# Kernel optimization log

Measured on AMD Instinct MI355X. Metric: run time of the kernel, lower is better.

The kernel has to match this reference:

```python
import jax, jax.numpy as jnp
import numpy as np

EPS = 1e-8  # torch F.cosine_similarity eps
TEMP = 2.0  # hardcoded in module regardless of init arg


def _normalize(x):
    # row-normalize with torch-style eps clamp on the norm
    norm = jnp.sqrt(jnp.sum(x * x, axis=-1, keepdims=True))
    return x / jnp.maximum(norm, EPS)


def setup_inputs() -> dict:
    key = jax.random.key(0)
    k1, k2, k3 = jax.random.split(key, 3)
    n, m, d = 8192, 8192, 256
    return {
        "pos_key": jax.random.normal(k1, (n, d), dtype=jnp.float32),
        "pos_value": jax.random.normal(k2, (n, d), dtype=jnp.float32),
        "neg_value": jax.random.normal(k3, (m, d), dtype=jnp.float32),
    }


def reference(pos_key, pos_value, neg_value):
    pk = _normalize(pos_key)    # [n, d]
    pv = _normalize(pos_value)  # [n, d]
    nv = _normalize(neg_value)  # [m, d]

    pos_sim = jnp.sum(pk * pv, axis=-1)          # [n]
    neg_sim = jnp.einsum("nd,md->nm", pk, nv)    # [n, m] cosine sims

    pos_loss = -jnp.mean(pos_sim / TEMP)
    # log-sum-exp over m (stable), matching log(sum(exp(.)))
    neg_loss = jnp.mean(jax.scipy.special.logsumexp(neg_sim / TEMP, axis=-1))
    return pos_loss + neg_loss
```

## Files before the change

### kernel.cpp

```cpp
#include <hip/hip_runtime.h>

typedef __attribute__((ext_vector_type(4))) float f32x4;
typedef __attribute__((ext_vector_type(4))) int   i32x4;
typedef __attribute__((ext_vector_type(8))) int   i32x8;

#define DIM 256
#define D4  64

#define GLD_LDS16(g, l) __builtin_amdgcn_global_load_lds(                      \
    (const __attribute__((address_space(1))) void*)(g),                        \
    (__attribute__((address_space(3))) void*)(l), 16, 0, 0)

__global__ __launch_bounds__(256) void normalize_kernel(
    const float4* __restrict__ pk, const float4* __restrict__ pv,
    const float4* __restrict__ nv, unsigned int* __restrict__ pkn,
    unsigned int* __restrict__ nvn, float* __restrict__ posPart, int N) {
  int row  = blockIdx.x * 4 + (threadIdx.x >> 6);
  int lane = threadIdx.x & 63;
  if (row < N) {
    float4 x = pk[row * D4 + lane];
    float4 y = pv[row * D4 + lane];
    float skk = x.x*x.x + x.y*x.y + x.z*x.z + x.w*x.w;
    float svv = y.x*y.x + y.y*y.y + y.z*y.z + y.w*y.w;
    float skv = x.x*y.x + x.y*y.y + x.z*y.z + x.w*y.w;
#pragma unroll
    for (int m = 32; m >= 1; m >>= 1) {
      skk += __shfl_xor(skk, m, 64);
      svv += __shfl_xor(svv, m, 64);
      skv += __shfl_xor(skv, m, 64);
    }
    float nk  = fmaxf(sqrtf(skk), 1e-8f);
    float nvv = fmaxf(sqrtf(svv), 1e-8f);
    if (lane == 0) posPart[row] = skv / (nk * nvv);
    float rk = 1.0f / nk;
    int w = __builtin_amdgcn_cvt_pk_fp8_f32(x.x * rk, x.y * rk, 0, false);
    w = __builtin_amdgcn_cvt_pk_fp8_f32(x.z * rk, x.w * rk, w, true);
    pkn[(size_t)row * 64 + lane] = (unsigned int)w;
  } else {
    int r2 = row - N;
    float4 x = nv[r2 * D4 + lane];
    float s = x.x*x.x + x.y*x.y + x.z*x.z + x.w*x.w;
#pragma unroll
    for (int m = 32; m >= 1; m >>= 1) s += __shfl_xor(s, m, 64);
    float rn = 1.0f / fmaxf(sqrtf(s), 1e-8f);
    int w = __builtin_amdgcn_cvt_pk_fp8_f32(x.x * rn, x.y * rn, 0, false);
    w = __builtin_amdgcn_cvt_pk_fp8_f32(x.z * rn, x.w * rn, w, true);
    nvn[(size_t)r2 * 64 + lane] = (unsigned int)w;
  }
}

__global__ __launch_bounds__(256, 3) void gemm_lse_kernel(
    const unsigned char* __restrict__ gA, const unsigned char* __restrict__ gB,
    float* __restrict__ partial, int N) {
  __shared__ unsigned char As[16384];
  __shared__ unsigned char Bs[16384];

  const int tid  = threadIdx.x;
  const int lane = tid & 63;
  const int wv   = tid >> 6;
  const int wm   = wv >> 1, wn = wv & 1;
  const int l15  = lane & 15, q = lane >> 4;
  const int row0 = blockIdx.y * 128;
  const int col0 = blockIdx.x * 128;
  const float kLog2eHalf = 0.72134752044448170f;
  const int kUnitScale = 0x7F7F7F7F;

  f32x4 acc[4][4];
#pragma unroll
  for (int mi = 0; mi < 4; mi++)
#pragma unroll
    for (int ni = 0; ni < 4; ni++) acc[mi][ni] = (f32x4){0.f, 0.f, 0.f, 0.f};

#pragma unroll
  for (int kb = 0; kb < 2; kb++) {
    if (kb) __syncthreads();
#pragma unroll
    for (int i = 0; i < 4; i++) {
      int c  = i * 256 + tid;
      int r  = c >> 3;
      int sc = ((c & 7) ^ (r & 7)) << 4;
      GLD_LDS16(gA + (size_t)(row0 + r) * 256 + kb * 128 + sc, As + c * 16);
      GLD_LDS16(gB + (size_t)(col0 + r) * 256 + kb * 128 + sc, Bs + c * 16);
    }
    __syncthreads();

    i32x8 bf[4];
#pragma unroll
    for (int ni = 0; ni < 4; ni++) {
      int r  = wn * 64 + ni * 16 + l15;
      int c0 = (q * 2)     ^ (r & 7);
      int c1 = (q * 2 + 1) ^ (r & 7);
      i32x4 lo = *(const i32x4*)(Bs + r * 128 + c0 * 16);
      i32x4 hi = *(const i32x4*)(Bs + r * 128 + c1 * 16);
      bf[ni] = (i32x8){lo.x, lo.y, lo.z, lo.w, hi.x, hi.y, hi.z, hi.w};
    }
#pragma unroll
    for (int mi = 0; mi < 4; mi++) {
      int r  = wm * 64 + mi * 16 + l15;
      int c0 = (q * 2)     ^ (r & 7);
      int c1 = (q * 2 + 1) ^ (r & 7);
      i32x4 lo = *(const i32x4*)(As + r * 128 + c0 * 16);
      i32x4 hi = *(const i32x4*)(As + r * 128 + c1 * 16);
      i32x8 af = (i32x8){lo.x, lo.y, lo.z, lo.w, hi.x, hi.y, hi.z, hi.w};
#pragma unroll
      for (int ni = 0; ni < 4; ni++)
        acc[mi][ni] = __builtin_amdgcn_mfma_scale_f32_16x16x128_f8f6f4(
            af, bf[ni], acc[mi][ni],
            0, 0, 0, kUnitScale, 0, kUnitScale);
    }
  }

  float keep = 0.f;
#pragma unroll
  for (int mi = 0; mi < 4; mi++)
#pragma unroll
    for (int rr = 0; rr < 4; rr++) {
      float v = 0.f;
#pragma unroll
      for (int ni = 0; ni < 4; ni++)
        v += __builtin_amdgcn_exp2f(acc[mi][ni][rr] * kLog2eHalf);
      v += __shfl_xor(v, 1, 16);
      v += __shfl_xor(v, 2, 16);
      v += __shfl_xor(v, 4, 16);
      v += __shfl_xor(v, 8, 16);
      if (l15 == mi * 4 + rr) keep = v;
    }
  int lrow = (l15 >> 2) * 16 + q * 4 + (l15 & 3);
  partial[(size_t)(blockIdx.x * 2 + wn) * N + row0 + wm * 64 + lrow] = keep;
}

__global__ __launch_bounds__(256) void finalize_kernel(
    const float* __restrict__ partial, const float* __restrict__ posPart,
    float* __restrict__ out, int N, int slabsPerGroup, float invN) {
  __shared__ float red[4][64];
  int t  = threadIdx.x;
  int rl = t & 63, g = t >> 6;
  int row = blockIdx.x * 64 + rl;
  const float* p = partial + (size_t)(g * slabsPerGroup) * N + row;
  float s = 0.f;
#pragma unroll 8
  for (int j = 0; j < slabsPerGroup; j++) s += p[(size_t)j * N];
  red[g][rl] = s;
  __syncthreads();
  if (t < 64) {
    float tot = red[0][rl] + red[1][rl] + red[2][rl] + red[3][rl];
    float v = __builtin_amdgcn_logf(tot) * 0.69314718055994531f
              - 0.5f * posPart[row];
#pragma unroll
    for (int m = 32; m >= 1; m >>= 1) v += __shfl_xor(v, m, 64);
    if (rl == 0) atomicAdd(out, v * invN);
  }
}

extern "C" void kernel_launch(void* const* d_in, const int* in_sizes, int n_in,
                              void* d_out, int out_size, void* d_ws, size_t ws_size,
                              hipStream_t stream) {
  const float* pk = (const float*)d_in[0];
  const float* pv = (const float*)d_in[1];
  const float* nv = (const float*)d_in[2];
  int N = in_sizes[0] / DIM;
  int M = in_sizes[2] / DIM;
  float* out = (float*)d_out;

  unsigned char* pkn = (unsigned char*)d_ws;
  unsigned char* nvn = pkn + (size_t)N * DIM;
  float* partial = (float*)(nvn + (size_t)M * DIM);
  float* posPart = partial + (size_t)(M / 64) * N;

  hipMemsetAsync(out, 0, sizeof(float), stream);

  normalize_kernel<<<(N + M) / 4, 256, 0, stream>>>(
      (const float4*)pk, (const float4*)pv, (const float4*)nv,
      (unsigned int*)pkn, (unsigned int*)nvn, posPart, N);

  gemm_lse_kernel<<<dim3(M / 128, N / 128), 256, 0, stream>>>(
      pkn, nvn, partial, N);

  finalize_kernel<<<N / 64, 256, 0, stream>>>(
      partial, posPart, out, N, (M / 64) / 4, 1.0f / (float)N);
}
```

Before: 106.9 us.

## Load GEMM fragments directly from global into registers, bypassing LDS

The GEMM kernel stops staging A and B tiles through shared memory with global_load_lds and barriers. Each wave now loads its own MFMA fragments straight from global memory into registers, issuing all loads for both K halves up front. This removes the LDS round trip and the block-level syncs. In exchange, operands shared between waves are fetched from global or cache once per wave instead of once per block, and register pressure rises, so the occupancy hint drops from 3 to 2.

```diff
diff --git a/kernel.cpp b/kernel.cpp
--- a/kernel.cpp
+++ b/kernel.cpp
@@ -6,10 +6,6 @@
 
 #define DIM 256
 #define D4  64
-
-#define GLD_LDS16(g, l) __builtin_amdgcn_global_load_lds(                      \
-    (const __attribute__((address_space(1))) void*)(g),                        \
-    (__attribute__((address_space(3))) void*)(l), 16, 0, 0)
 
 __global__ __launch_bounds__(256) void normalize_kernel(
     const float4* __restrict__ pk, const float4* __restrict__ pv,
@@ -49,21 +45,32 @@
   }
 }
 
-__global__ __launch_bounds__(256, 3) void gemm_lse_kernel(
+__global__ __launch_bounds__(256, 2) void gemm_lse_kernel(
     const unsigned char* __restrict__ gA, const unsigned char* __restrict__ gB,
     float* __restrict__ partial, int N) {
-  __shared__ unsigned char As[16384];
-  __shared__ unsigned char Bs[16384];
-
   const int tid  = threadIdx.x;
   const int lane = tid & 63;
   const int wv   = tid >> 6;
   const int wm   = wv >> 1, wn = wv & 1;
   const int l15  = lane & 15, q = lane >> 4;
-  const int row0 = blockIdx.y * 128;
-  const int col0 = blockIdx.x * 128;
+  const int row0 = blockIdx.y * 128 + wm * 64;
+  const int col0 = blockIdx.x * 128 + wn * 64;
   const float kLog2eHalf = 0.72134752044448170f;
   const int kUnitScale = 0x7F7F7F7F;
+
+  const unsigned char* pa = gA + (size_t)(row0 + l15) * 256 + q * 32;
+  const unsigned char* pb = gB + (size_t)(col0 + l15) * 256 + q * 32;
+
+  i32x4 alo[2][4], ahi[2][4], blo[2][4], bhi[2][4];
+#pragma unroll
+  for (int kb = 0; kb < 2; kb++)
+#pragma unroll
+    for (int i = 0; i < 4; i++) {
+      alo[kb][i] = *(const i32x4*)(pa + i * 4096 + kb * 128);
+      ahi[kb][i] = *(const i32x4*)(pa + i * 4096 + kb * 128 + 16);
+      blo[kb][i] = *(const i32x4*)(pb + i * 4096 + kb * 128);
+      bhi[kb][i] = *(const i32x4*)(pb + i * 4096 + kb * 128 + 16);
+    }
 
   f32x4 acc[4][4];
 #pragma unroll
@@ -73,40 +80,21 @@
 
 #pragma unroll
   for (int kb = 0; kb < 2; kb++) {
-    if (kb) __syncthreads();
-#pragma unroll
-    for (int i = 0; i < 4; i++) {
-      int c  = i * 256 + tid;
-      int r  = c >> 3;
-      int sc = ((c & 7) ^ (r & 7)) << 4;
-      GLD_LDS16(gA + (size_t)(row0 + r) * 256 + kb * 128 + sc, As + c * 16);
-      GLD_LDS16(gB + (size_t)(col0 + r) * 256 + kb * 128 + sc, Bs + c * 16);
-    }
-    __syncthreads();
-
     i32x8 bf[4];
 #pragma unroll
-    for (int ni = 0; ni < 4; ni++) {
-      int r  = wn * 64 + ni * 16 + l15;
-      int c0 = (q * 2)     ^ (r & 7);
-      int c1 = (q * 2 + 1) ^ (r & 7);
-      i32x4 lo = *(const i32x4*)(Bs + r * 128 + c0 * 16);
-      i32x4 hi = *(const i32x4*)(Bs + r * 128 + c1 * 16);
-      bf[ni] = (i32x8){lo.x, lo.y, lo.z, lo.w, hi.x, hi.y, hi.z, hi.w};
-    }
+    for (int ni = 0; ni < 4; ni++)
+      bf[ni] = (i32x8){blo[kb][ni].x, blo[kb][ni].y, blo[kb][ni].z, blo[kb][ni].w,
+                       bhi[kb][ni].x, bhi[kb][ni].y, bhi[kb][ni].z, bhi[kb][ni].w};
 #pragma unroll
     for (int mi = 0; mi < 4; mi++) {
-      int r  = wm * 64 + mi * 16 + l15;
-      int c0 = (q * 2)     ^ (r & 7);
-      int c1 = (q * 2 + 1) ^ (r & 7);
-      i32x4 lo = *(const i32x4*)(As + r * 128 + c0 * 16);
-      i32x4 hi = *(const i32x4*)(As + r * 128 + c1 * 16);
-      i32x8 af = (i32x8){lo.x, lo.y, lo.z, lo.w, hi.x, hi.y, hi.z, hi.w};
+      i32x8 af = (i32x8){alo[kb][mi].x, alo[kb][mi].y, alo[kb][mi].z, alo[kb][mi].w,
+                         ahi[kb][mi].x, ahi[kb][mi].y, ahi[kb][mi].z, ahi[kb][mi].w};
 #pragma unroll
       for (int ni = 0; ni < 4; ni++)
         acc[mi][ni] = __builtin_amdgcn_mfma_scale_f32_16x16x128_f8f6f4(
             af, bf[ni], acc[mi][ni],
-            0, 0, 0, kUnitScale, 0, kUnitScale);
+            0, 0,
+            0, kUnitScale, 0, kUnitScale);
     }
   }
 
@@ -126,7 +114,7 @@
       if (l15 == mi * 4 + rr) keep = v;
     }
   int lrow = (l15 >> 2) * 16 + q * 4 + (l15 & 3);
-  partial[(size_t)(blockIdx.x * 2 + wn) * N + row0 + wm * 64 + lrow] = keep;
+  partial[(size_t)(blockIdx.x * 2 + wn) * N + (row0 - wm * 64) + wm * 64 + lrow] = keep;
 }
 
 __global__ __launch_bounds__(256) void finalize_kernel(
```

Result: slower. 138.4 us (+29.5%).
